# Kernel optimization log

Hardware: AMD Instinct MI355X
Metric: run time of the kernel (lower is better)

## Reference

```python
import jax, jax.numpy as jnp
import numpy as np

GRID_SIZE = 5
SPLINE_ORDER = 3
GRID_LO, GRID_HI = -1.0, 1.0
N_BASIS = GRID_SIZE + SPLINE_ORDER  # 8


def make_grid():
    # Extended knot vector as in efficient-kan: grid_size+2*spline_order+1 points
    h = (GRID_HI - GRID_LO) / GRID_SIZE
    return (jnp.arange(-SPLINE_ORDER, GRID_SIZE + SPLINE_ORDER + 1, dtype=jnp.float32) * h + GRID_LO)  # (12,)


def b_splines(x, grid):
    # Cox-de Boor recursion; x: (...,) -> (..., N_BASIS)
    xg = x[..., None]
    bases = ((xg >= grid[:-1]) & (xg < grid[1:])).astype(x.dtype)
    for k in range(1, SPLINE_ORDER + 1):
        left = (xg - grid[: -(k + 1)]) / (grid[k:-1] - grid[: -(k + 1)]) * bases[..., :-1]
        right = (grid[k + 1:] - xg) / (grid[k + 1:] - grid[1:-k]) * bases[..., 1:]
        bases = left + right
    return bases


def extract_patches3(x):
    # x: (B, C, H, W) -> (B, C, 9, H, W); 3x3 kernel, stride 1, padding 1
    B, C, H, W = x.shape
    xp = jnp.pad(x, ((0, 0), (0, 0), (1, 1), (1, 1)))
    return jnp.stack([xp[:, :, di:di + H, dj:dj + W]
                      for di in range(3) for dj in range(3)], axis=2)


def kan_conv(x, base_w, spline_w, scaler, grid):
    # One KANLinear(9 -> 1) per (out_ch, in_ch) pair, summed over in_ch.
    p = extract_patches3(x)                          # (B, Cin, 9, H, W)
    base = jnp.einsum('biphw,oip->bohw', jax.nn.silu(p), base_w)
    basis = b_splines(p, grid)                       # (B, Cin, 9, H, W, G)
    sw = spline_w * scaler[..., None]                # standalone spline scaler
    spl = jnp.einsum('biphwg,oipg->bohw', basis, sw)
    return base + spl


def maxpool2(x):
    B, C, H, W = x.shape
    return x.reshape(B, C, H // 2, 2, W // 2, 2).max(axis=(3, 5))


def setup_inputs() -> dict:
    key = jax.random.key(0)
    ks = jax.random.split(key, 7)
    return {
        'x': jax.random.normal(ks[0], (2048, 1, 28, 28), dtype=jnp.float32),
        'base_w1': jax.random.normal(ks[1], (2, 1, 9), dtype=jnp.float32) * 0.3,
        'spline_w1': jax.random.normal(ks[2], (2, 1, 9, 8), dtype=jnp.float32) * 0.1,
        'scaler1': jax.random.normal(ks[3], (2, 1, 9), dtype=jnp.float32) * 0.3 + 1.0,
        'base_w2': jax.random.normal(ks[4], (2, 2, 9), dtype=jnp.float32) * 0.3,
        'spline_w2': jax.random.normal(ks[5], (2, 2, 9, 8), dtype=jnp.float32) * 0.1,
        'scaler2': jax.random.normal(ks[6], (2, 2, 9), dtype=jnp.float32) * 0.3 + 1.0,
    }


def reference(x, base_w1, spline_w1, scaler1, base_w2, spline_w2, scaler2):
    grid = make_grid()
    h = maxpool2(kan_conv(x, base_w1, spline_w1, scaler1, grid))   # (B, 2, 14, 14)
    h = maxpool2(kan_conv(h, base_w2, spline_w2, scaler2, grid))   # (B, 2, 7, 7)
    return h.reshape(h.shape[0], -1)                               # (B, 98)
```

## Files before the change

### kernel.cpp

```cpp
#include <hip/hip_runtime.h>
#include <math.h>

typedef _Float16 half_t;
typedef _Float16 h2 __attribute__((ext_vector_type(2)));
typedef unsigned int uint;
typedef unsigned long long u64;

#define TPB 256

__device__ __forceinline__ uint pack_h2f(float a, float b) {
  half_t ha = (half_t)a, hb = (half_t)b;
  unsigned short ua = __builtin_bit_cast(unsigned short, ha);
  unsigned short ub = __builtin_bit_cast(unsigned short, hb);
  return (uint)ua | ((uint)ub << 16);
}

__device__ __forceinline__ float dot8v(uint d0, uint d1, uint d2, uint d3,
                                       float sv, uint4 wa, uint wb, float acc) {
  acc = fmaf(sv, __uint_as_float(wb), acc);
#if __has_builtin(__builtin_amdgcn_fdot2)
  acc = __builtin_amdgcn_fdot2(__builtin_bit_cast(h2, d0), __builtin_bit_cast(h2, wa.x), acc, false);
  acc = __builtin_amdgcn_fdot2(__builtin_bit_cast(h2, d1), __builtin_bit_cast(h2, wa.y), acc, false);
  acc = __builtin_amdgcn_fdot2(__builtin_bit_cast(h2, d2), __builtin_bit_cast(h2, wa.z), acc, false);
  acc = __builtin_amdgcn_fdot2(__builtin_bit_cast(h2, d3), __builtin_bit_cast(h2, wa.w), acc, false);
#else
  uint dd[4] = {d0, d1, d2, d3};
  uint ww[4] = {wa.x, wa.y, wa.z, wa.w};
#pragma unroll
  for (int k = 0; k < 4; ++k) {
    h2 f = __builtin_bit_cast(h2, dd[k]);
    h2 wv = __builtin_bit_cast(h2, ww[k]);
    acc = fmaf((float)f.x, (float)wv.x, acc);
    acc = fmaf((float)f.y, (float)wv.y, acc);
  }
#endif
  return acc;
}

__device__ __forceinline__ void feat_store(float x, uint* __restrict__ A,
                                           uint* __restrict__ Bq,
                                           uint* __restrict__ S) {
  float e = __expf(-x);
  float silu = x * __builtin_amdgcn_rcpf(1.0f + e);
  float s = fmaf(x, 2.5f, 5.5f);
  float sf = floorf(s);
  float t = s - sf;
  int p = (int)sf - 3;
  float omt = 1.0f - t, t2 = t * t;
  float B0 = (1.0f / 6.0f) * omt * omt * omt;
  float B3 = (1.0f / 6.0f) * t2 * t;
  float B1 = fmaf(0.5f * t, t2, 2.0f / 3.0f - t2);
  float B2 = 1.0f - B0 - B1 - B3;
  u64 Av = ((u64)pack_h2f(B2, B3) << 32) | pack_h2f(B0, B1);
  int n = p < 0 ? -p : 0;
  Av = (n >= 4) ? 0ull : (Av >> (16 * n));
  int pc = p < 0 ? 0 : (p > 9 ? 9 : p);
  int sh = 16 * pc;
  u64 lo = (sh < 64) ? (Av << sh) : 0ull;
  u64 hi = (sh == 0) ? 0ull
         : (sh < 64) ? (Av >> (64 - sh))
         : (sh < 128) ? (Av << (sh - 64)) : 0ull;
  *(uint2*)A = make_uint2((uint)lo, (uint)(lo >> 32));
  *(uint2*)Bq = make_uint2((uint)hi, (uint)(hi >> 32));
  *S = __float_as_uint(silu);
}

__device__ __forceinline__ float s1_load(const float* __restrict__ xb, int ii,
                                         int& sidx) {
  int hp = ii >= 450 ? 1 : 0;
  int k = ii - hp * 450;
  int r = k / 15, cc = k % 15;
  int c = 2 * cc + hp;
  bool inter = ((uint)(r - 1) < 28u) && ((uint)(c - 1) < 28u);
  int xi = (r - 1) * 28 + (c - 1);
  xi = min(max(xi, 0), 783);
  float xv = xb[xi];
  sidx = r * 30 + cc + hp * 15;
  return inter ? xv : 0.0f;
}

__global__ void pack_w(const float* __restrict__ bw1, const float* __restrict__ sw1,
                       const float* __restrict__ sc1, const float* __restrict__ bw2,
                       const float* __restrict__ sw2, const float* __restrict__ sc2,
                       uint* __restrict__ W) {
  const int t = threadIdx.x;
  if (t < 18) {
    const float scv = sc1[t];
    uint* dst = W + t * 8;
#pragma unroll
    for (int j = 0; j < 4; ++j)
      dst[j] = pack_h2f(sw1[t * 8 + 2 * j] * scv, sw1[t * 8 + 2 * j + 1] * scv);
    dst[4] = __float_as_uint(bw1[t]);
  } else if (t < 54) {
    const int q = t - 18;
    const float scv = sc2[q];
    uint* dst = W + t * 8;
#pragma unroll
    for (int j = 0; j < 4; ++j)
      dst[j] = pack_h2f(sw2[q * 8 + 2 * j] * scv, sw2[q * 8 + 2 * j + 1] * scv);
    dst[4] = __float_as_uint(bw2[q]);
  }
}

__global__ __launch_bounds__(TPB, 6) void kan_fwd(
    const float* __restrict__ x, const uint* __restrict__ W,
    float* __restrict__ out)
{
  __shared__ __align__(16) uint lds[6460];
  uint* F1A = lds;
  uint* F1B = lds + 1800;
  uint* F1S = lds + 3600;
  uint* F2A = lds + 4500;
  uint* F2B = lds + 5284;
  uint* F2S = lds + 6068;
  float* P = (float*)lds;

  const int tid = threadIdx.x;
  const float* xb = x + (size_t)blockIdx.x * 784;

  {
    int s0, s1i, s2i, s3i;
    const bool has3 = tid < (900 - 768);
    float x0 = s1_load(xb, tid, s0);
    float x1 = s1_load(xb, tid + 256, s1i);
    float x2 = s1_load(xb, tid + 512, s2i);
    float x3 = s1_load(xb, has3 ? tid + 768 : tid, s3i);
    feat_store(x0, F1A + s0 * 2, F1B + s0 * 2, F1S + s0);
    feat_store(x1, F1A + s1i * 2, F1B + s1i * 2, F1S + s1i);
    feat_store(x2, F1A + s2i * 2, F1B + s2i * 2, F1S + s2i);
    if (has3) feat_store(x3, F1A + s3i * 2, F1B + s3i * 2, F1S + s3i);
  }
  __syncthreads();

  if (tid < 196) {
    const int ph = tid / 14, pw = tid % 14;
    float acc[2][4];
#pragma unroll
    for (int o = 0; o < 2; ++o)
#pragma unroll
      for (int q = 0; q < 4; ++q) acc[o][q] = 0.0f;
#pragma unroll
    for (int r = 0; r < 4; ++r) {
#pragma unroll
      for (int c = 0; c < 4; ++c) {
        const int sidx = (2 * ph + r) * 30 + (pw + (c >> 1)) + (c & 1) * 15;
        uint2 a = *(const uint2*)(F1A + sidx * 2);
        uint2 bq = *(const uint2*)(F1B + sidx * 2);
        float sv = __uint_as_float(F1S[sidx]);
#pragma unroll
        for (int dh = 0; dh < 2; ++dh) {
          if (r - dh < 0 || r - dh > 2) continue;
#pragma unroll
          for (int dw = 0; dw < 2; ++dw) {
            if (c - dw < 0 || c - dw > 2) continue;
            const int tap = (r - dh) * 3 + (c - dw);
#pragma unroll
            for (int o = 0; o < 2; ++o) {
              const uint4 wa = *(const uint4*)(W + (o * 9 + tap) * 8);
              const uint wb = W[(o * 9 + tap) * 8 + 4];
              acc[o][dh * 2 + dw] =
                  dot8v(a.x, a.y, bq.x, bq.y, sv, wa, wb, acc[o][dh * 2 + dw]);
            }
          }
        }
      }
    }
#pragma unroll
    for (int o = 0; o < 2; ++o) {
      float m = fmaxf(fmaxf(acc[o][0], acc[o][1]), fmaxf(acc[o][2], acc[o][3]));
      int fidx = o * 196 + ph * 14 + (pw >> 1) + (pw & 1) * 7;
      feat_store(m, F2A + fidx * 2, F2B + fidx * 2, F2S + fidx);
    }
  }
  __syncthreads();

  {
    const int wid = __builtin_amdgcn_readfirstlane(tid >> 6);
    const int lane = tid & 63;
    const uint F0d1 = pack_h2f(1.0f / 48.0f, 23.0f / 48.0f);
    const uint F0d2 = pack_h2f(23.0f / 48.0f, 1.0f / 48.0f);
    if (lane < 49) {
      const int ci = wid & 1;
      const int ph = lane / 7, pw = lane % 7;
      float pa[4] = {0.0f, 0.0f, 0.0f, 0.0f};
#pragma unroll
      for (int r = 0; r < 4; ++r) {
#pragma unroll
        for (int c = 0; c < 4; ++c) {
          int row = 2 * ph + r - 1, col = 2 * pw + c - 1;
          bool ok = ((uint)row < 14u) && ((uint)col < 14u);
          int rcl = min(max(row, 0), 13), ccl = min(max(col, 0), 13);
          const int fidx = ci * 196 + rcl * 14 + (ccl >> 1) + (ccl & 1) * 7;
          uint2 a = *(const uint2*)(F2A + fidx * 2);
          uint2 bq = *(const uint2*)(F2B + fidx * 2);
          float sv = ok ? __uint_as_float(F2S[fidx]) : 0.0f;
          uint d0 = ok ? a.x : 0u;
          uint d1 = ok ? a.y : F0d1;
          uint d2 = ok ? bq.x : F0d2;
          uint d3 = ok ? bq.y : 0u;
#pragma unroll
          for (int dh = 0; dh < 2; ++dh) {
            if (r - dh < 0 || r - dh > 2) continue;
#pragma unroll
            for (int dw = 0; dw < 2; ++dw) {
              if (c - dw < 0 || c - dw > 2) continue;
              const int tap = (r - dh) * 3 + (c - dw);
              const uint4 wa = *(const uint4*)(W + (18 + wid * 9 + tap) * 8);
              const uint wb = W[(18 + wid * 9 + tap) * 8 + 4];
              pa[dh * 2 + dw] =
                  dot8v(d0, d1, d2, d3, sv, wa, wb, pa[dh * 2 + dw]);
            }
          }
        }
      }
      *(float4*)&P[(wid * 49 + lane) * 4] = make_float4(pa[0], pa[1], pa[2], pa[3]);
    }
  }
  __syncthreads();

  if (tid < 98) {
    const int o = tid / 49, pos = tid % 49;
    const float4 p0 = *(const float4*)&P[((o * 2 + 0) * 49 + pos) * 4];
    const float4 p1 = *(const float4*)&P[((o * 2 + 1) * 49 + pos) * 4];
    float m = fmaxf(fmaxf(p0.x + p1.x, p0.y + p1.y), fmaxf(p0.z + p1.z, p0.w + p1.w));
    out[(size_t)blockIdx.x * 98 + tid] = m;
  }
}

extern "C" void kernel_launch(void* const* d_in, const int* in_sizes, int n_in,
                              void* d_out, int out_size, void* d_ws, size_t ws_size,
                              hipStream_t stream) {
  const float* x   = (const float*)d_in[0];
  const float* bw1 = (const float*)d_in[1];
  const float* sw1 = (const float*)d_in[2];
  const float* sc1 = (const float*)d_in[3];
  const float* bw2 = (const float*)d_in[4];
  const float* sw2 = (const float*)d_in[5];
  const float* sc2 = (const float*)d_in[6];
  float* out = (float*)d_out;
  uint* W = (uint*)d_ws;
  const int B = in_sizes[0] / 784;
  pack_w<<<1, 64, 0, stream>>>(bw1, sw1, sc1, bw2, sw2, sc2, W);
  kan_fwd<<<B, TPB, 0, stream>>>(x, W, out);
}
```

Baseline: 93.58 us.

## Recompute stage-1 features in registers instead of staging them through LDS

Stage 1 no longer precomputes spline/SiLU features for the padded 30x30 input into shared memory. Each of the 196 pooled-output threads now loads its 4x4 input window from global memory and computes the features in registers, so the first barrier and the large LDS buffer go away. LDS use drops enough to raise launch bounds from 6 to 8 blocks per CU. The cost is redundant work: each input pixel's feature is computed up to four times, and only 196 of 256 threads do it, where the old code spread the work over all threads.

```diff
diff --git a/kernel.cpp b/kernel.cpp
--- a/kernel.cpp
+++ b/kernel.cpp
@@ -37,11 +37,10 @@
   return acc;
 }
 
-__device__ __forceinline__ void feat_store(float x, uint* __restrict__ A,
-                                           uint* __restrict__ Bq,
-                                           uint* __restrict__ S) {
+__device__ __forceinline__ void feat_reg(float x, uint& d0, uint& d1,
+                                         uint& d2, uint& d3, float& sv) {
   float e = __expf(-x);
-  float silu = x * __builtin_amdgcn_rcpf(1.0f + e);
+  sv = x * __builtin_amdgcn_rcpf(1.0f + e);
   float s = fmaf(x, 2.5f, 5.5f);
   float sf = floorf(s);
   float t = s - sf;
@@ -60,23 +59,18 @@
   u64 hi = (sh == 0) ? 0ull
          : (sh < 64) ? (Av >> (64 - sh))
          : (sh < 128) ? (Av << (sh - 64)) : 0ull;
-  *(uint2*)A = make_uint2((uint)lo, (uint)(lo >> 32));
-  *(uint2*)Bq = make_uint2((uint)hi, (uint)(hi >> 32));
-  *S = __float_as_uint(silu);
-}
-
-__device__ __forceinline__ float s1_load(const float* __restrict__ xb, int ii,
-                                         int& sidx) {
-  int hp = ii >= 450 ? 1 : 0;
-  int k = ii - hp * 450;
-  int r = k / 15, cc = k % 15;
-  int c = 2 * cc + hp;
-  bool inter = ((uint)(r - 1) < 28u) && ((uint)(c - 1) < 28u);
-  int xi = (r - 1) * 28 + (c - 1);
-  xi = min(max(xi, 0), 783);
-  float xv = xb[xi];
-  sidx = r * 30 + cc + hp * 15;
-  return inter ? xv : 0.0f;
+  d0 = (uint)lo; d1 = (uint)(lo >> 32);
+  d2 = (uint)hi; d3 = (uint)(hi >> 32);
+}
+
+__device__ __forceinline__ void feat_store(float x, uint* __restrict__ A,
+                                           uint* __restrict__ Bq,
+                                           uint* __restrict__ S) {
+  uint d0, d1, d2, d3; float sv;
+  feat_reg(x, d0, d1, d2, d3, sv);
+  *(uint2*)A = make_uint2(d0, d1);
+  *(uint2*)Bq = make_uint2(d2, d3);
+  *S = __float_as_uint(sv);
 }
 
 __global__ void pack_w(const float* __restrict__ bw1, const float* __restrict__ sw1,
@@ -102,38 +96,34 @@
   }
 }
 
-__global__ __launch_bounds__(TPB, 6) void kan_fwd(
+__global__ __launch_bounds__(TPB, 8) void kan_fwd(
     const float* __restrict__ x, const uint* __restrict__ W,
     float* __restrict__ out)
 {
-  __shared__ __align__(16) uint lds[6460];
-  uint* F1A = lds;
-  uint* F1B = lds + 1800;
-  uint* F1S = lds + 3600;
-  uint* F2A = lds + 4500;
-  uint* F2B = lds + 5284;
-  uint* F2S = lds + 6068;
-  float* P = (float*)lds;
+  __shared__ __align__(16) uint lds[2744];
+  uint* F2A = lds;
+  uint* F2B = lds + 784;
+  uint* F2S = lds + 1568;
+  float* P = (float*)(lds + 1960);
 
   const int tid = threadIdx.x;
   const float* xb = x + (size_t)blockIdx.x * 784;
 
-  {
-    int s0, s1i, s2i, s3i;
-    const bool has3 = tid < (900 - 768);
-    float x0 = s1_load(xb, tid, s0);
-    float x1 = s1_load(xb, tid + 256, s1i);
-    float x2 = s1_load(xb, tid + 512, s2i);
-    float x3 = s1_load(xb, has3 ? tid + 768 : tid, s3i);
-    feat_store(x0, F1A + s0 * 2, F1B + s0 * 2, F1S + s0);
-    feat_store(x1, F1A + s1i * 2, F1B + s1i * 2, F1S + s1i);
-    feat_store(x2, F1A + s2i * 2, F1B + s2i * 2, F1S + s2i);
-    if (has3) feat_store(x3, F1A + s3i * 2, F1B + s3i * 2, F1S + s3i);
-  }
-  __syncthreads();
-
   if (tid < 196) {
     const int ph = tid / 14, pw = tid % 14;
+    float xv[16];
+#pragma unroll
+    for (int r = 0; r < 4; ++r) {
+      const int row = 2 * ph + r - 1;
+#pragma unroll
+      for (int c = 0; c < 4; ++c) {
+        const int col = 2 * pw + c - 1;
+        const bool ok = ((uint)row < 28u) && ((uint)col < 28u);
+        const int xi = min(max(row, 0), 27) * 28 + min(max(col, 0), 27);
+        float v = xb[xi];
+        xv[r * 4 + c] = ok ? v : 0.0f;
+      }
+    }
     float acc[2][4];
 #pragma unroll
     for (int o = 0; o < 2; ++o)
@@ -143,10 +133,8 @@
     for (int r = 0; r < 4; ++r) {
 #pragma unroll
       for (int c = 0; c < 4; ++c) {
-        const int sidx = (2 * ph + r) * 30 + (pw + (c >> 1)) + (c & 1) * 15;
-        uint2 a = *(const uint2*)(F1A + sidx * 2);
-        uint2 bq = *(const uint2*)(F1B + sidx * 2);
-        float sv = __uint_as_float(F1S[sidx]);
+        uint d0, d1, d2, d3; float sv;
+        feat_reg(xv[r * 4 + c], d0, d1, d2, d3, sv);
 #pragma unroll
         for (int dh = 0; dh < 2; ++dh) {
           if (r - dh < 0 || r - dh > 2) continue;
@@ -159,7 +147,7 @@
               const uint4 wa = *(const uint4*)(W + (o * 9 + tap) * 8);
               const uint wb = W[(o * 9 + tap) * 8 + 4];
               acc[o][dh * 2 + dw] =
-                  dot8v(a.x, a.y, bq.x, bq.y, sv, wa, wb, acc[o][dh * 2 + dw]);
+                  dot8v(d0, d1, d2, d3, sv, wa, wb, acc[o][dh * 2 + dw]);
             }
           }
         }
```

After: 182.2 us. 1.95x slower.
